# Kernel tuning notes

Measured on AMD Instinct MI355X. Metric: run time of the kernel, lower is better.

Reference implementation:

```python
import jax, jax.numpy as jnp
import numpy as np

B, T, D = 2, 2048, 1024
H, RANK = 16, 16
HD = D // H  # 64


def setup_inputs() -> dict:
    key = jax.random.key(0)
    ks = jax.random.split(key, 10)
    x = jax.random.normal(ks[0], (B, T, D), dtype=jnp.float32)
    def lin(k):
        kw, kb = jax.random.split(k)
        W = jax.random.normal(kw, (D, D), dtype=jnp.float32) * (1.0 / np.sqrt(D))
        b = jax.random.normal(kb, (D,), dtype=jnp.float32) * 0.01
        return W, b
    Wq, bq = lin(ks[1])
    Wk, bk = lin(ks[2])
    Wv, bv = lin(ks[3])
    Wo, bo = lin(ks[4])
    # per-head low-rank metric factors A_h: (min(rank, head_dim), head_dim)
    A = jax.random.normal(ks[5], (H, min(RANK, HD), HD), dtype=jnp.float32) * 0.02
    log_lambda = jnp.full((H,), jnp.log(jnp.float32(0.1)), dtype=jnp.float32)
    return {"x": x, "Wq": Wq, "bq": bq, "Wk": Wk, "bk": bk,
            "Wv": Wv, "bv": bv, "Wo": Wo, "bo": bo,
            "A": A, "log_lambda": log_lambda}


def reference(x, Wq, bq, Wk, bk, Wv, bv, Wo, bo, A, log_lambda):
    b, t, d = x.shape
    h = A.shape[0]
    hd = d // h

    def split_heads(y):
        return y.reshape(b, t, h, hd).transpose(0, 2, 1, 3)  # (b,h,t,hd)

    q = split_heads(x @ Wq.T + bq)
    k = split_heads(x @ Wk.T + bk)
    v = split_heads(x @ Wv.T + bv)

    # Metric g_h = A_h^T A_h + lam_h * I. torch.einsum('btid,dd,btjd->btj')
    # uses only diag(g) and sums over i: dist[b,t,j] = sum_d S[b,t,d]*gdiag[d]*diff[b,t,j,d]
    # where S[b,t,d] = sum_i (q[b,t,d] - k[b,i,d]) = t*q - sum_i k.
    gdiag = jnp.sum(A * A, axis=1) + jnp.exp(log_lambda)[:, None]  # (h,hd)

    ksum = jnp.sum(k, axis=2)                      # (b,h,hd)
    S = jnp.float32(t) * q - ksum[:, :, None, :]   # (b,h,t,hd)
    Sg = S * gdiag[None, :, None, :]               # (b,h,t,hd)
    c = jnp.sum(Sg * q, axis=-1)                   # (b,h,t)
    # dist_sq[b,h,t,j] = c[b,h,t] - sum_d Sg[b,h,t,d] * k[b,h,j,d]
    dist_sq = c[..., None] - jnp.einsum('bhtd,bhjd->bhtj', Sg, k)
    attn = jax.nn.softmax(-dist_sq, axis=-1)       # (b,h,t,t)
    o = jnp.einsum('bhtj,bhjd->bhtd', attn, v)     # (b,h,t,hd)
    out = o.transpose(0, 2, 1, 3).reshape(b, t, d)
    return out @ Wo.T + bo
```

## Files before the change

kernel.cpp:

```cpp
#include <hip/hip_runtime.h>
#include <math.h>

#define D_MODEL 1024
#define NHEAD   16
#define HDIM    64
#define SEQ     2048
#define BATCH   2
#define NROWS   (BATCH*SEQ)

typedef unsigned short u16;
typedef __attribute__((ext_vector_type(4))) unsigned short u16x4;
typedef __attribute__((ext_vector_type(8))) short short8;
typedef __attribute__((ext_vector_type(4))) float f32x4;
typedef __attribute__((ext_vector_type(2))) unsigned int u32x2;

__device__ __forceinline__ u16 f2bf(float x) {
    unsigned int u = __float_as_uint(x);
    u += 0x7fffu + ((u >> 16) & 1u);
    return (u16)(u >> 16);
}
__device__ __forceinline__ float bf2f(u16 h) {
    return __uint_as_float(((unsigned int)h) << 16);
}
__device__ __forceinline__ unsigned int cvt_pk_bf16(float a, float b) {
    unsigned int r;
    asm("v_cvt_pk_bf16_f32 %0, %1, %2" : "=v"(r) : "v"(a), "v"(b));
    return r;
}
__device__ __forceinline__ short8 ld8(const u16* p) {
    u16x4 a = *(const u16x4*)p;
    u16x4 b = *(const u16x4*)(p + 4);
    short8 r;
    r[0]=(short)a[0]; r[1]=(short)a[1]; r[2]=(short)a[2]; r[3]=(short)a[3];
    r[4]=(short)b[0]; r[5]=(short)b[1]; r[6]=(short)b[2]; r[7]=(short)b[3];
    return r;
}
__device__ __forceinline__ void st8(u16* p, short8 v) {
    u16x4 a, b;
    a[0]=(u16)v[0]; a[1]=(u16)v[1]; a[2]=(u16)v[2]; a[3]=(u16)v[3];
    b[0]=(u16)v[4]; b[1]=(u16)v[5]; b[2]=(u16)v[6]; b[3]=(u16)v[7];
    *(u16x4*)p = a; *(u16x4*)(p + 4) = b;
}

__global__ void gdiag_kernel(const float* __restrict__ A,
                             const float* __restrict__ log_lambda,
                             float* __restrict__ gdiag) {
    int id = blockIdx.x * 256 + threadIdx.x;
    if (id >= NHEAD * HDIM) return;
    int h = id >> 6, d = id & 63;
    float s = 0.f;
#pragma unroll
    for (int i = 0; i < 16; ++i) {
        float a = A[(h * 16 + i) * HDIM + d];
        s += a * a;
    }
    gdiag[id] = (s + __expf(log_lambda[h])) * 1.4426950408889634f;
}

__global__ void prep_split(const float* __restrict__ x,
                           const float* __restrict__ Wq, const float* __restrict__ Wk,
                           const float* __restrict__ Wv, const float* __restrict__ Wo,
                           u16* __restrict__ xh, u16* __restrict__ xl,
                           u16* __restrict__ wqh, u16* __restrict__ wql,
                           u16* __restrict__ wkh, u16* __restrict__ wkl,
                           u16* __restrict__ wvh, u16* __restrict__ woh) {
    int seg = blockIdx.y;
    int i = blockIdx.x * 256 + threadIdx.x;
    const float* src; u16* dh; u16* dl; int n4;
    if      (seg == 0) { src = x;  dh = xh;  dl = xl;      n4 = NROWS * D_MODEL / 4; }
    else if (seg == 1) { src = Wq; dh = wqh; dl = wql;     n4 = D_MODEL * D_MODEL / 4; }
    else if (seg == 2) { src = Wk; dh = wkh; dl = wkl;     n4 = D_MODEL * D_MODEL / 4; }
    else if (seg == 3) { src = Wv; dh = wvh; dl = nullptr; n4 = D_MODEL * D_MODEL / 4; }
    else               { src = Wo; dh = woh; dl = nullptr; n4 = D_MODEL * D_MODEL / 4; }
    if (i >= n4) return;
    float4 v = *(const float4*)&src[(size_t)i * 4];
    float vv[4] = {v.x, v.y, v.z, v.w};
    u16x4 hv, lv;
#pragma unroll
    for (int j = 0; j < 4; ++j) {
        u16 hb = f2bf(vv[j]);
        hv[j] = hb;
        lv[j] = f2bf(vv[j] - bf2f(hb));
    }
    *(u16x4*)&dh[(size_t)i * 4] = hv;
    if (dl) *(u16x4*)&dl[(size_t)i * 4] = lv;
}

template<int NP3>
__global__ __launch_bounds__(256)
void gemm_mfma(const u16* __restrict__ Ah, const u16* __restrict__ Al,
               const u16* __restrict__ BhA, const u16* __restrict__ BlA, const float* __restrict__ biasA,
               float* outfA, u16* auxhA, u16* auxlA, float* ksumA,
               const u16* __restrict__ BhB, const u16* __restrict__ BlB, const float* __restrict__ biasB,
               float* outfB, u16* auxhB, u16* auxlB, float* ksumB,
               int out_layout) {
    const int z = blockIdx.z;
    const u16* Bh = (z == 0) ? BhA : BhB;
    const u16* Bl = (z == 0) ? BlA : BlB;
    const float* bias = (z == 0) ? biasA : biasB;
    float* outf = (z == 0) ? outfA : outfB;
    u16* auxh   = (z == 0) ? auxhA : auxhB;
    u16* auxl   = (z == 0) ? auxlA : auxlB;
    float* ksump= (z == 0) ? ksumA : ksumB;

    __shared__ u16 As_h[128][36], Bs_h[128][36];
    __shared__ u16 As_l[128][36], Bs_l[128][36];

    const int tid = threadIdx.x;
    const int w = tid >> 6, lane = tid & 63, quad = lane >> 4, n16 = lane & 15;
    const int rBase = blockIdx.y * 128;
    const int cBase = blockIdx.x * 128;

    f32x4 acc[2][8] = {};

    for (int kt = 0; kt < D_MODEL; kt += 32) {
#pragma unroll
        for (int s = 0; s < 2; ++s) {
            int id = s * 256 + tid;
            int row = id >> 2;
            int c8 = (id & 3) * 8;
            st8(&As_h[row][c8], *(const short8*)&Ah[(size_t)(rBase + row) * D_MODEL + kt + c8]);
            st8(&Bs_h[row][c8], *(const short8*)&Bh[(size_t)(cBase + row) * D_MODEL + kt + c8]);
            if (NP3) {
                st8(&As_l[row][c8], *(const short8*)&Al[(size_t)(rBase + row) * D_MODEL + kt + c8]);
                st8(&Bs_l[row][c8], *(const short8*)&Bl[(size_t)(cBase + row) * D_MODEL + kt + c8]);
            }
        }
        __syncthreads();

        short8 a_h[2], a_l[2];
#pragma unroll
        for (int mt = 0; mt < 2; ++mt) {
            a_h[mt] = ld8(&As_h[w * 32 + mt * 16 + n16][quad * 8]);
            if (NP3) a_l[mt] = ld8(&As_l[w * 32 + mt * 16 + n16][quad * 8]);
        }
#pragma unroll
        for (int nt = 0; nt < 8; ++nt) {
            short8 b_h = ld8(&Bs_h[nt * 16 + n16][quad * 8]);
            short8 b_l;
            if (NP3) b_l = ld8(&Bs_l[nt * 16 + n16][quad * 8]);
#pragma unroll
            for (int mt = 0; mt < 2; ++mt) {
                acc[mt][nt] = __builtin_amdgcn_mfma_f32_16x16x32_bf16(a_h[mt], b_h, acc[mt][nt], 0, 0, 0);
                if (NP3) {
                    acc[mt][nt] = __builtin_amdgcn_mfma_f32_16x16x32_bf16(a_h[mt], b_l, acc[mt][nt], 0, 0, 0);
                    acc[mt][nt] = __builtin_amdgcn_mfma_f32_16x16x32_bf16(a_l[mt], b_h, acc[mt][nt], 0, 0, 0);
                }
            }
        }
        __syncthreads();
    }

    float csum[8];
#pragma unroll
    for (int nt = 0; nt < 8; ++nt) csum[nt] = 0.f;
#pragma unroll
    for (int mt = 0; mt < 2; ++mt) {
#pragma unroll
        for (int nt = 0; nt < 8; ++nt) {
            int c = cBase + nt * 16 + n16;
            float bc = bias[c];
            int rb = rBase + w * 32 + mt * 16 + quad * 4;
#pragma unroll
            for (int reg = 0; reg < 4; ++reg) {
                float val = acc[mt][nt][reg] + bc;
                int rr = rb + reg;
                size_t idx = out_layout
                    ? ((size_t)(((rr >> 11) * NHEAD + (c >> 6)) * SEQ + (rr & (SEQ - 1)))) * HDIM + (c & 63)
                    : (size_t)rr * D_MODEL + c;
                if (outf) outf[idx] = val;
                if (auxh) {
                    u16 hb = f2bf(val);
                    auxh[idx] = hb;
                    if (auxl) auxl[idx] = f2bf(val - bf2f(hb));
                }
                csum[nt] += val;
            }
        }
    }
    if (ksump) {
#pragma unroll
        for (int nt = 0; nt < 8; ++nt) {
            float cs = csum[nt];
            cs += __shfl_xor(cs, 16);
            cs += __shfl_xor(cs, 32);
            if (quad == 0) {
                int c = cBase + nt * 16 + n16;
                int bb = rBase >> 11;
                atomicAdd(&ksump[(bb * NHEAD + (c >> 6)) * HDIM + (c & 63)], cs);
            }
        }
    }
}

__global__ __launch_bounds__(256)
void vtrans_kernel(const u16* __restrict__ vh, u16* __restrict__ vT) {
    __shared__ u16 tile[64][72];
    const int tid = threadIdx.x;
    const int t0 = blockIdx.x * 64;
    const int bh = blockIdx.y;
    const u16* vp = vh + (size_t)bh * SEQ * HDIM;
#pragma unroll
    for (int s = 0; s < 2; ++s) {
        int id = s * 256 + tid;
        int row = id >> 3, c8 = (id & 7) * 8;
        st8(&tile[row][c8], *(const short8*)&vp[(size_t)(t0 + row) * HDIM + c8]);
    }
    __syncthreads();
#pragma unroll
    for (int s = 0; s < 2; ++s) {
        int id = s * 256 + tid;
        int d = id >> 3, t8 = (id & 7) * 8;
        short8 r;
#pragma unroll
        for (int i = 0; i < 8; ++i) r[i] = (short)tile[t8 + i][d];
        *(short8*)&vT[((size_t)bh * HDIM + d) * SEQ + t0 + t8] = r;
    }
}

__global__ __launch_bounds__(256, 4)
void flash_mfma(const float* __restrict__ q, const u16* __restrict__ kh,
                const u16* __restrict__ kl, const u16* __restrict__ vT,
                const float* __restrict__ ksum, const float* __restrict__ gdiag,
                u16* __restrict__ o) {
    __shared__ __align__(16) u16 khs[64][72], kls[64][72], vTs[64][72];
    __shared__ __align__(16) u16 ps[4][16][72];

    const int tid = threadIdx.x;
    const int w = tid >> 6, lane = tid & 63, quad = lane >> 4, n16 = lane & 15;
    const int t0 = blockIdx.x * 64;
    const int h = blockIdx.y, b = blockIdx.z;
    const size_t bh = (size_t)b * NHEAD + h;
    const float* qp = q + bh * SEQ * HDIM;
    const u16* khp = kh + bh * SEQ * HDIM;
    const u16* klp = kl + bh * SEQ * HDIM;
    const u16* vtp = vT + bh * HDIM * SEQ;

    short8 sgh[2], sgl[2];
    {
        int qrow = t0 + w * 16 + n16;
#pragma unroll
        for (int kc = 0; kc < 2; ++kc) {
            int d0 = kc * 32 + quad * 8;
            float4 q0 = *(const float4*)&qp[(size_t)qrow * HDIM + d0];
            float4 q1 = *(const float4*)&qp[(size_t)qrow * HDIM + d0 + 4];
            float4 k0 = *(const float4*)&ksum[bh * HDIM + d0];
            float4 k1 = *(const float4*)&ksum[bh * HDIM + d0 + 4];
            float4 g0 = *(const float4*)&gdiag[(size_t)h * HDIM + d0];
            float4 g1 = *(const float4*)&gdiag[(size_t)h * HDIM + d0 + 4];
            float sg[8];
            sg[0] = (2048.f * q0.x - k0.x) * g0.x; sg[1] = (2048.f * q0.y - k0.y) * g0.y;
            sg[2] = (2048.f * q0.z - k0.z) * g0.z; sg[3] = (2048.f * q0.w - k0.w) * g0.w;
            sg[4] = (2048.f * q1.x - k1.x) * g1.x; sg[5] = (2048.f * q1.y - k1.y) * g1.y;
            sg[6] = (2048.f * q1.z - k1.z) * g1.z; sg[7] = (2048.f * q1.w - k1.w) * g1.w;
#pragma unroll
            for (int j = 0; j < 8; ++j) {
                u16 hb = f2bf(sg[j]);
                sgh[kc][j] = (short)hb;
                sgl[kc][j] = (short)f2bf(sg[j] - bf2f(hb));
            }
        }
    }

    f32x4 oaccv[4] = {};
    float m_n = -INFINITY, l_n = 0.f;

    const int srow = tid >> 3;
    const int sc8  = (tid & 7) * 8;

    short8 rk0h = *(const short8*)&khp[(size_t)srow * HDIM + sc8];
    short8 rk1h = *(const short8*)&khp[(size_t)(srow + 32) * HDIM + sc8];
    short8 rk0l = *(const short8*)&klp[(size_t)srow * HDIM + sc8];
    short8 rk1l = *(const short8*)&klp[(size_t)(srow + 32) * HDIM + sc8];
    short8 rv0  = *(const short8*)&vtp[(size_t)srow * SEQ + sc8];
    short8 rv1  = *(const short8*)&vtp[(size_t)(srow + 32) * SEQ + sc8];
    *(short8*)&khs[srow][sc8] = rk0h;  *(short8*)&khs[srow + 32][sc8] = rk1h;
    *(short8*)&kls[srow][sc8] = rk0l;  *(short8*)&kls[srow + 32][sc8] = rk1l;
    *(short8*)&vTs[srow][sc8] = rv0;   *(short8*)&vTs[srow + 32][sc8] = rv1;
    __syncthreads();

    for (int j0 = 0; j0 < SEQ; j0 += 64) {
        const int jn = j0 + 64;
        const bool pf = (jn < SEQ);
        if (pf) {
            rk0h = *(const short8*)&khp[(size_t)(jn + srow) * HDIM + sc8];
            rk1h = *(const short8*)&khp[(size_t)(jn + srow + 32) * HDIM + sc8];
            rk0l = *(const short8*)&klp[(size_t)(jn + srow) * HDIM + sc8];
            rk1l = *(const short8*)&klp[(size_t)(jn + srow + 32) * HDIM + sc8];
            rv0  = *(const short8*)&vtp[(size_t)srow * SEQ + jn + sc8];
            rv1  = *(const short8*)&vtp[(size_t)(srow + 32) * SEQ + jn + sc8];
        }

        f32x4 lgT[4] = {};
#pragma unroll
        for (int kc = 0; kc < 2; ++kc) {
#pragma unroll
            for (int nt = 0; nt < 4; ++nt) {
                short8 b_h = *(const short8*)&khs[nt * 16 + n16][kc * 32 + quad * 8];
                short8 b_l = *(const short8*)&kls[nt * 16 + n16][kc * 32 + quad * 8];
                lgT[nt] = __builtin_amdgcn_mfma_f32_16x16x32_bf16(b_h, sgh[kc], lgT[nt], 0, 0, 0);
                lgT[nt] = __builtin_amdgcn_mfma_f32_16x16x32_bf16(b_l, sgh[kc], lgT[nt], 0, 0, 0);
                lgT[nt] = __builtin_amdgcn_mfma_f32_16x16x32_bf16(b_h, sgl[kc], lgT[nt], 0, 0, 0);
            }
        }

        float mx = fmaxf(fmaxf(fmaxf(lgT[0][0], lgT[0][1]), fmaxf(lgT[0][2], lgT[0][3])),
                         fmaxf(fmaxf(lgT[1][0], lgT[1][1]), fmaxf(lgT[1][2], lgT[1][3])));
        mx = fmaxf(mx, fmaxf(fmaxf(fmaxf(lgT[2][0], lgT[2][1]), fmaxf(lgT[2][2], lgT[2][3])),
                             fmaxf(fmaxf(lgT[3][0], lgT[3][1]), fmaxf(lgT[3][2], lgT[3][3]))));
        mx = fmaxf(mx, __shfl_xor(mx, 16));
        mx = fmaxf(mx, __shfl_xor(mx, 32));
        const float mn = fmaxf(m_n, mx);
        const float alpha = exp2f(m_n - mn);
        m_n = mn;

        float psum = 0.f;
#pragma unroll
        for (int nt = 0; nt < 4; ++nt) {
#pragma unroll
            for (int r = 0; r < 4; ++r) lgT[nt][r] = exp2f(lgT[nt][r] - mn);
            u32x2 pk;
            pk[0] = cvt_pk_bf16(lgT[nt][0], lgT[nt][1]);
            pk[1] = cvt_pk_bf16(lgT[nt][2], lgT[nt][3]);
            *(u32x2*)&ps[w][n16][nt * 16 + quad * 4] = pk;
            psum += (lgT[nt][0] + lgT[nt][1]) + (lgT[nt][2] + lgT[nt][3]);
        }
        psum += __shfl_xor(psum, 16);
        psum += __shfl_xor(psum, 32);
        l_n = l_n * alpha + psum;

        const float a0 = __shfl(alpha, quad * 4 + 0);
        const float a1 = __shfl(alpha, quad * 4 + 1);
        const float a2 = __shfl(alpha, quad * 4 + 2);
        const float a3 = __shfl(alpha, quad * 4 + 3);
#pragma unroll
        for (int nt = 0; nt < 4; ++nt) {
            oaccv[nt][0] *= a0; oaccv[nt][1] *= a1;
            oaccv[nt][2] *= a2; oaccv[nt][3] *= a3;
        }

        short8 pa0 = *(const short8*)&ps[w][n16][quad * 8];
        short8 pa1 = *(const short8*)&ps[w][n16][32 + quad * 8];
#pragma unroll
        for (int nt = 0; nt < 4; ++nt) {
            short8 v0 = *(const short8*)&vTs[nt * 16 + n16][quad * 8];
            short8 v1 = *(const short8*)&vTs[nt * 16 + n16][32 + quad * 8];
            oaccv[nt] = __builtin_amdgcn_mfma_f32_16x16x32_bf16(pa0, v0, oaccv[nt], 0, 0, 0);
            oaccv[nt] = __builtin_amdgcn_mfma_f32_16x16x32_bf16(pa1, v1, oaccv[nt], 0, 0, 0);
        }
        __syncthreads();
        if (pf) {
            *(short8*)&khs[srow][sc8] = rk0h;  *(short8*)&khs[srow + 32][sc8] = rk1h;
            *(short8*)&kls[srow][sc8] = rk0l;  *(short8*)&kls[srow + 32][sc8] = rk1l;
            *(short8*)&vTs[srow][sc8] = rv0;   *(short8*)&vTs[srow + 32][sc8] = rv1;
            __syncthreads();
        }
    }

#pragma unroll
    for (int r = 0; r < 4; ++r) {
        float lr = __shfl(l_n, quad * 4 + r);
        float inv = 1.f / lr;
        int t = t0 + w * 16 + quad * 4 + r;
#pragma unroll
        for (int nt = 0; nt < 4; ++nt) {
            int d = nt * 16 + n16;
            o[((size_t)(b * SEQ + t)) * D_MODEL + h * HDIM + d] = f2bf(oaccv[nt][r] * inv);
        }
    }
}

extern "C" void kernel_launch(void* const* d_in, const int* in_sizes, int n_in,
                              void* d_out, int out_size, void* d_ws, size_t ws_size,
                              hipStream_t stream) {
    const float* x  = (const float*)d_in[0];
    const float* Wq = (const float*)d_in[1];
    const float* bq = (const float*)d_in[2];
    const float* Wk = (const float*)d_in[3];
    const float* bk = (const float*)d_in[4];
    const float* Wv = (const float*)d_in[5];
    const float* bv = (const float*)d_in[6];
    const float* Wo = (const float*)d_in[7];
    const float* bo = (const float*)d_in[8];
    const float* A  = (const float*)d_in[9];
    const float* ll = (const float*)d_in[10];
    float* out = (float*)d_out;

    const size_t NQKV = (size_t)NROWS * D_MODEL;
    const size_t NW = (size_t)D_MODEL * D_MODEL;
    char* base = (char*)d_ws;
    float* q_ws = (float*)base;            base += NQKV * 4;
    u16* xh  = (u16*)base;                 base += NQKV * 2;
    u16* xl  = (u16*)base;                 base += NQKV * 2;
    u16* khw = (u16*)base;                 base += NQKV * 2;
    u16* klw = (u16*)base;                 base += NQKV * 2;
    u16* vhw = (u16*)base;                 base += NQKV * 2;
    u16* wqh = (u16*)base;                 base += NW * 2;
    u16* wql = (u16*)base;                 base += NW * 2;
    u16* wkh = (u16*)base;                 base += NW * 2;
    u16* wkl = (u16*)base;                 base += NW * 2;
    u16* wvh = (u16*)base;                 base += NW * 2;
    u16* woh = (u16*)base;                 base += NW * 2;
    float* gd_ws   = (float*)base;         base += NHEAD * HDIM * 4;
    float* ksum_ws = (float*)base;         base += BATCH * NHEAD * HDIM * 4;

    hipMemsetAsync(ksum_ws, 0, BATCH * NHEAD * HDIM * sizeof(float), stream);

    prep_split<<<dim3(4096, 5), 256, 0, stream>>>(x, Wq, Wk, Wv, Wo,
                                                  xh, xl, wqh, wql, wkh, wkl, wvh, woh);
    gdiag_kernel<<<4, 256, 0, stream>>>(A, ll, gd_ws);

    gemm_mfma<1><<<dim3(8, 32, 2), 256, 0, stream>>>(
        xh, xl,
        wqh, wql, bq, q_ws, nullptr, nullptr, nullptr,
        wkh, wkl, bk, nullptr, khw, klw, ksum_ws,
        1);
    gemm_mfma<0><<<dim3(8, 32, 1), 256, 0, stream>>>(
        xh, nullptr,
        wvh, nullptr, bv, nullptr, vhw, nullptr, nullptr,
        wvh, nullptr, bv, nullptr, vhw, nullptr, nullptr,
        1);

    u16* vTw = xl;
    u16* ohw = xh;
    vtrans_kernel<<<dim3(SEQ / 64, BATCH * NHEAD), 256, 0, stream>>>(vhw, vTw);

    flash_mfma<<<dim3(SEQ / 64, NHEAD, BATCH), 256, 0, stream>>>(
        q_ws, khw, klw, vTw, ksum_ws, gd_ws, ohw);

    gemm_mfma<0><<<dim3(8, 32, 1), 256, 0, stream>>>(
        ohw, nullptr,
        woh, nullptr, bo, out, nullptr, nullptr, nullptr,
        woh, nullptr, bo, out, nullptr, nullptr, nullptr,
        0);
}
```

Before: 331.7 us.

## Process two query tiles per wave in flash kernel and XOR-swizzle LDS

Each wave now handles 32 query rows (two 16-row M tiles) instead of 16, so every K/V fragment read from shared memory feeds twice as many MFMAs. The block covers 128 queries and the grid halves. The shared-memory padding is replaced by an XOR swizzle to avoid bank conflicts, and launch bounds drop to 2 blocks per SM to allow more registers. The trade-off is fewer blocks (512) and higher register pressure, which lowers occupancy.

Result: faster. 323.8 us (-2.4%).

```diff
diff --git a/kernel.cpp b/kernel.cpp
--- a/kernel.cpp
+++ b/kernel.cpp
@@ -13,6 +13,8 @@
 typedef __attribute__((ext_vector_type(8))) short short8;
 typedef __attribute__((ext_vector_type(4))) float f32x4;
 typedef __attribute__((ext_vector_type(2))) unsigned int u32x2;
+
+#define SWZ(row, c) (((c) ^ ((row) & 7)) * 8)
 
 __device__ __forceinline__ u16 f2bf(float x) {
     unsigned int u = __float_as_uint(x);
@@ -218,17 +220,17 @@
     }
 }
 
-__global__ __launch_bounds__(256, 4)
+__global__ __launch_bounds__(256, 2)
 void flash_mfma(const float* __restrict__ q, const u16* __restrict__ kh,
                 const u16* __restrict__ kl, const u16* __restrict__ vT,
                 const float* __restrict__ ksum, const float* __restrict__ gdiag,
                 u16* __restrict__ o) {
-    __shared__ __align__(16) u16 khs[64][72], kls[64][72], vTs[64][72];
-    __shared__ __align__(16) u16 ps[4][16][72];
+    __shared__ __align__(16) u16 khs[64][64], kls[64][64], vTs[64][64];
+    __shared__ __align__(16) u16 ps[4][32][64];
 
     const int tid = threadIdx.x;
     const int w = tid >> 6, lane = tid & 63, quad = lane >> 4, n16 = lane & 15;
-    const int t0 = blockIdx.x * 64;
+    const int t0 = blockIdx.x * 128;
     const int h = blockIdx.y, b = blockIdx.z;
     const size_t bh = (size_t)b * NHEAD + h;
     const float* qp = q + bh * SEQ * HDIM;
@@ -236,9 +238,10 @@
     const u16* klp = kl + bh * SEQ * HDIM;
     const u16* vtp = vT + bh * HDIM * SEQ;
 
-    short8 sgh[2], sgl[2];
-    {
-        int qrow = t0 + w * 16 + n16;
+    short8 sgh[2][2], sgl[2][2];
+#pragma unroll
+    for (int mt = 0; mt < 2; ++mt) {
+        int qrow = t0 + w * 32 + mt * 16 + n16;
 #pragma unroll
         for (int kc = 0; kc < 2; ++kc) {
             int d0 = kc * 32 + quad * 8;
@@ -256,116 +259,140 @@
 #pragma unroll
             for (int j = 0; j < 8; ++j) {
                 u16 hb = f2bf(sg[j]);
-                sgh[kc][j] = (short)hb;
-                sgl[kc][j] = (short)f2bf(sg[j] - bf2f(hb));
-            }
-        }
-    }
-
-    f32x4 oaccv[4] = {};
-    float m_n = -INFINITY, l_n = 0.f;
+                sgh[mt][kc][j] = (short)hb;
+                sgl[mt][kc][j] = (short)f2bf(sg[j] - bf2f(hb));
+            }
+        }
+    }
+
+    f32x4 oaccv[2][4] = {};
+    float m_n[2] = {-INFINITY, -INFINITY};
+    float l_n[2] = {0.f, 0.f};
 
     const int srow = tid >> 3;
-    const int sc8  = (tid & 7) * 8;
-
-    short8 rk0h = *(const short8*)&khp[(size_t)srow * HDIM + sc8];
-    short8 rk1h = *(const short8*)&khp[(size_t)(srow + 32) * HDIM + sc8];
-    short8 rk0l = *(const short8*)&klp[(size_t)srow * HDIM + sc8];
-    short8 rk1l = *(const short8*)&klp[(size_t)(srow + 32) * HDIM + sc8];
-    short8 rv0  = *(const short8*)&vtp[(size_t)srow * SEQ + sc8];
-    short8 rv1  = *(const short8*)&vtp[(size_t)(srow + 32) * SEQ + sc8];
-    *(short8*)&khs[srow][sc8] = rk0h;  *(short8*)&khs[srow + 32][sc8] = rk1h;
-    *(short8*)&kls[srow][sc8] = rk0l;  *(short8*)&kls[srow + 32][sc8] = rk1l;
-    *(short8*)&vTs[srow][sc8] = rv0;   *(short8*)&vTs[srow + 32][sc8] = rv1;
+    const int sc   = tid & 7;
+    const int scg  = sc * 8;
+    const int scl  = SWZ(srow, sc);
+
+    short8 rk0h = *(const short8*)&khp[(size_t)srow * HDIM + scg];
+    short8 rk1h = *(const short8*)&khp[(size_t)(srow + 32) * HDIM + scg];
+    short8 rk0l = *(const short8*)&klp[(size_t)srow * HDIM + scg];
+    short8 rk1l = *(const short8*)&klp[(size_t)(srow + 32) * HDIM + scg];
+    short8 rv0  = *(const short8*)&vtp[(size_t)srow * SEQ + scg];
+    short8 rv1  = *(const short8*)&vtp[(size_t)(srow + 32) * SEQ + scg];
+    *(short8*)&khs[srow][scl] = rk0h;  *(short8*)&khs[srow + 32][scl] = rk1h;
+    *(short8*)&kls[srow][scl] = rk0l;  *(short8*)&kls[srow + 32][scl] = rk1l;
+    *(short8*)&vTs[srow][scl] = rv0;   *(short8*)&vTs[srow + 32][scl] = rv1;
     __syncthreads();
 
     for (int j0 = 0; j0 < SEQ; j0 += 64) {
         const int jn = j0 + 64;
         const bool pf = (jn < SEQ);
         if (pf) {
-            rk0h = *(const short8*)&khp[(size_t)(jn + srow) * HDIM + sc8];
-            rk1h = *(const short8*)&khp[(size_t)(jn + srow + 32) * HDIM + sc8];
-            rk0l = *(const short8*)&klp[(size_t)(jn + srow) * HDIM + sc8];
-            rk1l = *(const short8*)&klp[(size_t)(jn + srow + 32) * HDIM + sc8];
-            rv0  = *(const short8*)&vtp[(size_t)srow * SEQ + jn + sc8];
-            rv1  = *(const short8*)&vtp[(size_t)(srow + 32) * SEQ + jn + sc8];
-        }
-
-        f32x4 lgT[4] = {};
+            rk0h = *(const short8*)&khp[(size_t)(jn + srow) * HDIM + scg];
+            rk1h = *(const short8*)&khp[(size_t)(jn + srow + 32) * HDIM + scg];
+            rk0l = *(const short8*)&klp[(size_t)(jn + srow) * HDIM + scg];
+            rk1l = *(const short8*)&klp[(size_t)(jn + srow + 32) * HDIM + scg];
+            rv0  = *(const short8*)&vtp[(size_t)srow * SEQ + jn + scg];
+            rv1  = *(const short8*)&vtp[(size_t)(srow + 32) * SEQ + jn + scg];
+        }
+
+        f32x4 lgT[2][4] = {};
 #pragma unroll
         for (int kc = 0; kc < 2; ++kc) {
 #pragma unroll
             for (int nt = 0; nt < 4; ++nt) {
-                short8 b_h = *(const short8*)&khs[nt * 16 + n16][kc * 32 + quad * 8];
-                short8 b_l = *(const short8*)&kls[nt * 16 + n16][kc * 32 + quad * 8];
-                lgT[nt] = __builtin_amdgcn_mfma_f32_16x16x32_bf16(b_h, sgh[kc], lgT[nt], 0, 0, 0);
-                lgT[nt] = __builtin_amdgcn_mfma_f32_16x16x32_bf16(b_l, sgh[kc], lgT[nt], 0, 0, 0);
-                lgT[nt] = __builtin_amdgcn_mfma_f32_16x16x32_bf16(b_h, sgl[kc], lgT[nt], 0, 0, 0);
-            }
-        }
-
-        float mx = fmaxf(fmaxf(fmaxf(lgT[0][0], lgT[0][1]), fmaxf(lgT[0][2], lgT[0][3])),
-                         fmaxf(fmaxf(lgT[1][0], lgT[1][1]), fmaxf(lgT[1][2], lgT[1][3])));
-        mx = fmaxf(mx, fmaxf(fmaxf(fmaxf(lgT[2][0], lgT[2][1]), fmaxf(lgT[2][2], lgT[2][3])),
-                             fmaxf(fmaxf(lgT[3][0], lgT[3][1]), fmaxf(lgT[3][2], lgT[3][3]))));
-        mx = fmaxf(mx, __shfl_xor(mx, 16));
-        mx = fmaxf(mx, __shfl_xor(mx, 32));
-        const float mn = fmaxf(m_n, mx);
-        const float alpha = exp2f(m_n - mn);
-        m_n = mn;
-
-        float psum = 0.f;
+                const int row = nt * 16 + n16;
+                const int cc = SWZ(row, kc * 4 + quad);
+                short8 b_h = *(const short8*)&khs[row][cc];
+                short8 b_l = *(const short8*)&kls[row][cc];
+#pragma unroll
+                for (int mt = 0; mt < 2; ++mt) {
+                    lgT[mt][nt] = __builtin_amdgcn_mfma_f32_16x16x32_bf16(b_h, sgh[mt][kc], lgT[mt][nt], 0, 0, 0);
+                    lgT[mt][nt] = __builtin_amdgcn_mfma_f32_16x16x32_bf16(b_l, sgh[mt][kc], lgT[mt][nt], 0, 0, 0);
+                    lgT[mt][nt] = __builtin_amdgcn_mfma_f32_16x16x32_bf16(b_h, sgl[mt][kc], lgT[mt][nt], 0, 0, 0);
+                }
+            }
+        }
+
+#pragma unroll
+        for (int mt = 0; mt < 2; ++mt) {
+            float mx = fmaxf(fmaxf(fmaxf(lgT[mt][0][0], lgT[mt][0][1]), fmaxf(lgT[mt][0][2], lgT[mt][0][3])),
+                             fmaxf(fmaxf(lgT[mt][1][0], lgT[mt][1][1]), fmaxf(lgT[mt][1][2], lgT[mt][1][3])));
+            mx = fmaxf(mx, fmaxf(fmaxf(fmaxf(lgT[mt][2][0], lgT[mt][2][1]), fmaxf(lgT[mt][2][2], lgT[mt][2][3])),
+                                 fmaxf(fmaxf(lgT[mt][3][0], lgT[mt][3][1]), fmaxf(lgT[mt][3][2], lgT[mt][3][3]))));
+            mx = fmaxf(mx, __shfl_xor(mx, 16));
+            mx = fmaxf(mx, __shfl_xor(mx, 32));
+            const float mn = fmaxf(m_n[mt], mx);
+            const float alpha = exp2f(m_n[mt] - mn);
+            m_n[mt] = mn;
+
+            const int prow = mt * 16 + n16;
+            float psum = 0.f;
+#pragma unroll
+            for (int nt = 0; nt < 4; ++nt) {
+#pragma unroll
+                for (int r = 0; r < 4; ++r) lgT[mt][nt][r] = exp2f(lgT[mt][nt][r] - mn);
+                u32x2 pk;
+                pk[0] = cvt_pk_bf16(lgT[mt][nt][0], lgT[mt][nt][1]);
+                pk[1] = cvt_pk_bf16(lgT[mt][nt][2], lgT[mt][nt][3]);
+                *(u32x2*)&ps[w][prow][SWZ(prow, nt * 2 + (quad >> 1)) + (quad & 1) * 4] = pk;
+                psum += (lgT[mt][nt][0] + lgT[mt][nt][1]) + (lgT[mt][nt][2] + lgT[mt][nt][3]);
+            }
+            psum += __shfl_xor(psum, 16);
+            psum += __shfl_xor(psum, 32);
+            l_n[mt] = l_n[mt] * alpha + psum;
+
+            const float a0 = __shfl(alpha, quad * 4 + 0);
+            const float a1 = __shfl(alpha, quad * 4 + 1);
+            const float a2 = __shfl(alpha, quad * 4 + 2);
+            const float a3 = __shfl(alpha, quad * 4 + 3);
+#pragma unroll
+            for (int nt = 0; nt < 4; ++nt) {
+                oaccv[mt][nt][0] *= a0; oaccv[mt][nt][1] *= a1;
+                oaccv[mt][nt][2] *= a2; oaccv[mt][nt][3] *= a3;
+            }
+        }
+
+        short8 pa[2][2];
+#pragma unroll
+        for (int mt = 0; mt < 2; ++mt) {
+            const int prow = mt * 16 + n16;
+            pa[mt][0] = *(const short8*)&ps[w][prow][SWZ(prow, quad)];
+            pa[mt][1] = *(const short8*)&ps[w][prow][SWZ(prow, quad + 4)];
+        }
 #pragma unroll
         for (int nt = 0; nt < 4; ++nt) {
-#pragma unroll
-            for (int r = 0; r < 4; ++r) lgT[nt][r] = exp2f(lgT[nt][r] - mn);
-            u32x2 pk;
-            pk[0] = cvt_pk_bf16(lgT[nt][0], lgT[nt][1]);
-            pk[1] = cvt_pk_bf16(lgT[nt][2], lgT[nt][3]);
-            *(u32x2*)&ps[w][n16][nt * 16 + quad * 4] = pk;
-            psum += (lgT[nt][0] + lgT[nt][1]) + (lgT[nt][2] + lgT[nt][3]);
-        }
-        psum += __shfl_xor(psum, 16);
-        psum += __shfl_xor(psum, 32);
-        l_n = l_n * alpha + psum;
-
-        const float a0 = __shfl(alpha, quad * 4 + 0);
-        const float a1 = __shfl(alpha, quad * 4 + 1);
-        const float a2 = __shfl(alpha, quad * 4 + 2);
-        const float a3 = __shfl(alpha, quad * 4 + 3);
-#pragma unroll
-        for (int nt = 0; nt < 4; ++nt) {
-            oaccv[nt][0] *= a0; oaccv[nt][1] *= a1;
-            oaccv[nt][2] *= a2; oaccv[nt][3] *= a3;
-        }
-
-        short8 pa0 = *(const short8*)&ps[w][n16][quad * 8];
-        short8 pa1 = *(const short8*)&ps[w][n16][32 + quad * 8];
-#pragma unroll
-        for (int nt = 0; nt < 4; ++nt) {
-            short8 v0 = *(const short8*)&vTs[nt * 16 + n16][quad * 8];
-            short8 v1 = *(const short8*)&vTs[nt * 16 + n16][32 + quad * 8];
-            oaccv[nt] = __builtin_amdgcn_mfma_f32_16x16x32_bf16(pa0, v0, oaccv[nt], 0, 0, 0);
-            oaccv[nt] = __builtin_amdgcn_mfma_f32_16x16x32_bf16(pa1, v1, oaccv[nt], 0, 0, 0);
+            const int row = nt * 16 + n16;
+            short8 v0 = *(const short8*)&vTs[row][SWZ(row, quad)];
+            short8 v1 = *(const short8*)&vTs[row][SWZ(row, quad + 4)];
+#pragma unroll
+            for (int mt = 0; mt < 2; ++mt) {
+                oaccv[mt][nt] = __builtin_amdgcn_mfma_f32_16x16x32_bf16(pa[mt][0], v0, oaccv[mt][nt], 0, 0, 0);
+                oaccv[mt][nt] = __builtin_amdgcn_mfma_f32_16x16x32_bf16(pa[mt][1], v1, oaccv[mt][nt], 0, 0, 0);
+            }
         }
         __syncthreads();
         if (pf) {
-            *(short8*)&khs[srow][sc8] = rk0h;  *(short8*)&khs[srow + 32][sc8] = rk1h;
-            *(short8*)&kls[srow][sc8] = rk0l;  *(short8*)&kls[srow + 32][sc8] = rk1l;
-            *(short8*)&vTs[srow][sc8] = rv0;   *(short8*)&vTs[srow + 32][sc8] = rv1;
+            *(short8*)&khs[srow][scl] = rk0h;  *(short8*)&khs[srow + 32][scl] = rk1h;
+            *(short8*)&kls[srow][scl] = rk0l;  *(short8*)&kls[srow + 32][scl] = rk1l;
+            *(short8*)&vTs[srow][scl] = rv0;   *(short8*)&vTs[srow + 32][scl] = rv1;
             __syncthreads();
         }
     }
 
 #pragma unroll
-    for (int r = 0; r < 4; ++r) {
-        float lr = __shfl(l_n, quad * 4 + r);
-        float inv = 1.f / lr;
-        int t = t0 + w * 16 + quad * 4 + r;
-#pragma unroll
-        for (int nt = 0; nt < 4; ++nt) {
-            int d = nt * 16 + n16;
-            o[((size_t)(b * SEQ + t)) * D_MODEL + h * HDIM + d] = f2bf(oaccv[nt][r] * inv);
+    for (int mt = 0; mt < 2; ++mt) {
+#pragma unroll
+        for (int r = 0; r < 4; ++r) {
+            float lr = __shfl(l_n[mt], quad * 4 + r);
+            float inv = 1.f / lr;
+            int t = t0 + w * 32 + mt * 16 + quad * 4 + r;
+#pragma unroll
+            for (int nt = 0; nt < 4; ++nt) {
+                int d = nt * 16 + n16;
+                o[((size_t)(b * SEQ + t)) * D_MODEL + h * HDIM + d] = f2bf(oaccv[mt][nt][r] * inv);
+            }
         }
     }
 }
@@ -425,7 +452,7 @@
     u16* ohw = xh;
     vtrans_kernel<<<dim3(SEQ / 64, BATCH * NHEAD), 256, 0, stream>>>(vhw, vTw);
 
-    flash_mfma<<<dim3(SEQ / 64, NHEAD, BATCH), 256, 0, stream>>>(
+    flash_mfma<<<dim3(SEQ / 128, NHEAD, BATCH), 256, 0, stream>>>(
         q_ws, khw, klw, vTw, ksum_ws, gd_ws, ohw);
 
     gemm_mfma<0><<<dim3(8, 32, 1), 256, 0, stream>>>(
```
